# Kernel tuning notes

Measured on AMD Instinct MI355X. Metric: run time of the kernel, lower is better.

## Reference

```python
import jax, jax.numpy as jnp
import numpy as np

HEAD_NUM = 16
KEY_DIM = 64
EMBED = 1024
KV_OUT = HEAD_NUM * KEY_DIM  # 1024


def setup_inputs() -> dict:
    key = jax.random.key(0)
    ks = jax.random.split(key, 11)
    B, L, E = 2, 2048, EMBED
    scale = 0.02
    return {
        "query": jax.random.normal(ks[0], (B, L, E), jnp.float32),
        "key": jax.random.normal(ks[1], (B, L, E), jnp.float32),
        "value": jax.random.normal(ks[2], (B, L, E), jnp.float32),
        "W_Query": jax.random.normal(ks[3], (E, KV_OUT), jnp.float32) * scale,
        "W_Key": jax.random.normal(ks[4], (E, KV_OUT), jnp.float32) * scale,
        "W_Value": jax.random.normal(ks[5], (E, KV_OUT), jnp.float32) * scale,
        "W_Output": jax.random.normal(ks[6], (KV_OUT, E), jnp.float32) * scale,
        "B_Query": jnp.zeros((KV_OUT,), jnp.float32),
        "B_Key": jnp.zeros((KV_OUT,), jnp.float32),
        "B_Value": jnp.zeros((KV_OUT,), jnp.float32),
        "B_Output": jnp.zeros((E,), jnp.float32),
    }


def reference(query, key, value, W_Query, W_Key, W_Value, W_Output,
              B_Query, B_Key, B_Value, B_Output):
    B, Lq, E = query.shape
    Lk = key.shape[1]
    H, D = HEAD_NUM, KEY_DIM
    # QKV projections + bias
    q = query @ W_Query + B_Query            # [B, Lq, H*D]
    k = key @ W_Key + B_Key                  # [B, Lk, H*D]
    v = value @ W_Value + B_Value            # [B, Lk, H*D]
    # tf.split(axis=2) per head == reshape to [B, L, H, D]
    q = q.reshape(B, Lq, H, D)
    k = k.reshape(B, Lk, H, D)
    v = v.reshape(B, Lk, H, D)
    # scaled dot-product attention (no mask, dropout=0)
    scores = jnp.einsum("bqhd,bkhd->bhqk", q, k) / (D ** 0.5)
    probs = jax.nn.softmax(scores, axis=-1)
    out = jnp.einsum("bhqk,bkhd->bqhd", probs, v)  # [B, Lq, H, D]
    out = out.reshape(B, Lq, H * D)
    return out @ W_Output + B_Output
```

## Files before the change

### kernel.cpp

```cpp
#include <hip/hip_runtime.h>

using u16 = unsigned short;
using u32 = unsigned int;

typedef __attribute__((ext_vector_type(8))) short bf16x8;
typedef __attribute__((ext_vector_type(4))) float f32x4;
typedef __attribute__((ext_vector_type(4))) u32 u32x4;
typedef __attribute__((ext_vector_type(2))) u32 u32x2;
typedef __attribute__((ext_vector_type(4))) _Float16 f16x4;

#define MFMA_BF16_K32(a, b, c) __builtin_amdgcn_mfma_f32_16x16x32_bf16((a), (b), (c), 0, 0, 0)
#define MFMA_F16_K16(a, b, c) __builtin_amdgcn_mfma_f32_16x16x16f16((a), (b), (c), 0, 0, 0)

#define QSCALE 0.18033688011112042f

extern "C" __device__ float __ocml_native_exp2_f32(float);

__device__ __forceinline__ u16 f2bf(float f) {
  u32 u = __builtin_bit_cast(u32, f);
  return (u16)((u + 0x7fffu + ((u >> 16) & 1u)) >> 16);
}

__device__ __forceinline__ u32 pk_f16(float a, float b) {
  auto v = __builtin_amdgcn_cvt_pkrtz(a, b);
  return __builtin_bit_cast(u32, v);
}

__device__ __forceinline__ void load_lds16(const void* g, void* l) {
  __builtin_amdgcn_global_load_lds((__attribute__((address_space(1))) void*)g,
                                   (__attribute__((address_space(3))) void*)l,
                                   16, 0, 0);
}

__global__ __launch_bounds__(256) void cvt_all_kernel(
    const float* __restrict__ q, const float* __restrict__ k, const float* __restrict__ v,
    u16* __restrict__ oq, u16* __restrict__ ok, u16* __restrict__ ov,
    const float* __restrict__ w0, const float* __restrict__ w1,
    const float* __restrict__ w2, const float* __restrict__ w3,
    u16* __restrict__ d0, u16* __restrict__ d1,
    u16* __restrict__ d2, u16* __restrict__ d3) {
  const int id = blockIdx.x;
  const int tid = threadIdx.x;
  if (id < 6144) {
    const int z = id >> 11, bx = id & 2047;
    const float* s = z == 0 ? q : z == 1 ? k : v;
    u16* d = z == 0 ? oq : z == 1 ? ok : ov;
    int i = (bx * 256 + tid) * 8;
    f32x4 a = *(const f32x4*)(s + i);
    f32x4 b = *(const f32x4*)(s + i + 4);
    u32x4 o;
    o.x = (u32)f2bf(a.x) | ((u32)f2bf(a.y) << 16);
    o.y = (u32)f2bf(a.z) | ((u32)f2bf(a.w) << 16);
    o.z = (u32)f2bf(b.x) | ((u32)f2bf(b.y) << 16);
    o.w = (u32)f2bf(b.z) | ((u32)f2bf(b.w) << 16);
    *(u32x4*)(d + i) = o;
    return;
  }
  __shared__ float t[64][65];
  const int r0 = id - 6144;
  const int z = r0 >> 8, rr0 = r0 & 255;
  const int bx = rr0 & 15, by = rr0 >> 4;
  const float* src = z == 0 ? w0 : z == 1 ? w1 : z == 2 ? w2 : w3;
  u16* dst = z == 0 ? d0 : z == 1 ? d1 : z == 2 ? d2 : d3;
  const float scale = (z == 0) ? QSCALE : 1.0f;
  const int r = tid >> 4, c4 = (tid & 15) * 4;
#pragma unroll
  for (int i = 0; i < 4; ++i) {
    int row = r + i * 16;
    f32x4 vv = *(const f32x4*)(src + (by * 64 + row) * 1024 + bx * 64 + c4);
    t[row][c4 + 0] = vv.x;
    t[row][c4 + 1] = vv.y;
    t[row][c4 + 2] = vv.z;
    t[row][c4 + 3] = vv.w;
  }
  __syncthreads();
  const int rw = tid >> 2, cc = (tid & 3) * 16;
  alignas(16) u16 tmp[16];
#pragma unroll
  for (int j = 0; j < 16; ++j) tmp[j] = f2bf(t[cc + j][rw] * scale);
  u32x4* outp = (u32x4*)(dst + (bx * 64 + rw) * 1024 + by * 64 + cc);
  outp[0] = *(const u32x4*)&tmp[0];
  outp[1] = *(const u32x4*)&tmp[8];
}

__global__ __launch_bounds__(256) void gemm_qkv_kernel(
    const u16* __restrict__ x0, const u16* __restrict__ x1, const u16* __restrict__ x2,
    const u16* __restrict__ w0, const u16* __restrict__ w1, const u16* __restrict__ w2,
    const float* __restrict__ b0, const float* __restrict__ b1, const float* __restrict__ b2,
    u16* __restrict__ c0, u16* __restrict__ c1, u16* __restrict__ vt) {
  __shared__ u16 As[128 * 64];
  __shared__ u16 Bs[128 * 64];
  const int z = blockIdx.z;
  const u16* A = z == 0 ? x0 : z == 1 ? x1 : x2;
  const u16* Bt = z == 0 ? w0 : z == 1 ? w1 : w2;
  const float* bias = z == 0 ? b0 : z == 1 ? b1 : b2;
  const float bscale = z == 0 ? QSCALE : 1.0f;
  const int tid = threadIdx.x;
  const int wave = tid >> 6, lane = tid & 63;
  const int l16 = lane & 15, quad = lane >> 4;
  const int wm = wave >> 1, wn = wave & 1;
  const int m0 = blockIdx.y * 128, n0 = blockIdx.x * 128;

  f32x4 acc[4][4];
  const f32x4 zf = {0.f, 0.f, 0.f, 0.f};
#pragma unroll
  for (int i = 0; i < 4; ++i)
#pragma unroll
    for (int j = 0; j < 4; ++j) acc[i][j] = zf;

  for (int kb = 0; kb < 1024; kb += 64) {
#pragma unroll
    for (int t = 0; t < 4; ++t) {
      int c = wave * 256 + t * 64 + lane;
      int row = c >> 3, c8 = c & 7;
      load_lds16(A + (m0 + row) * 1024 + kb + c8 * 8, &As[(wave * 256 + t * 64) * 8]);
    }
#pragma unroll
    for (int t = 0; t < 4; ++t) {
      int c = wave * 256 + t * 64 + lane;
      int row = c >> 3, c8 = c & 7;
      load_lds16(Bt + (n0 + row) * 1024 + kb + c8 * 8, &Bs[(wave * 256 + t * 64) * 8]);
    }
    asm volatile("s_waitcnt vmcnt(0)" ::: "memory");
    __syncthreads();
#pragma unroll
    for (int ks = 0; ks < 2; ++ks) {
      bf16x8 af[4], bfv[4];
#pragma unroll
      for (int mt = 0; mt < 4; ++mt)
        af[mt] = *(const bf16x8*)&As[(wm * 64 + mt * 16 + l16) * 64 + ks * 32 + quad * 8];
#pragma unroll
      for (int nt = 0; nt < 4; ++nt)
        bfv[nt] = *(const bf16x8*)&Bs[(wn * 64 + nt * 16 + l16) * 64 + ks * 32 + quad * 8];
#pragma unroll
      for (int mt = 0; mt < 4; ++mt)
#pragma unroll
        for (int nt = 0; nt < 4; ++nt) acc[mt][nt] = MFMA_BF16_K32(af[mt], bfv[nt], acc[mt][nt]);
    }
    __syncthreads();
  }

  float bv[4];
#pragma unroll
  for (int nt = 0; nt < 4; ++nt) bv[nt] = bias[n0 + wn * 64 + nt * 16 + l16] * bscale;
  if (z != 2) {
    u16* C = z == 0 ? c0 : c1;
#pragma unroll
    for (int mt = 0; mt < 4; ++mt)
#pragma unroll
      for (int nt = 0; nt < 4; ++nt)
#pragma unroll
        for (int r = 0; r < 4; ++r) {
          int row = m0 + wm * 64 + mt * 16 + quad * 4 + r;
          int col = n0 + wn * 64 + nt * 16 + l16;
          C[row * 1024 + col] = f2bf(acc[mt][nt][r] + bv[nt]);
        }
  } else {
#pragma unroll
    for (int mt = 0; mt < 4; ++mt)
#pragma unroll
      for (int nt = 0; nt < 4; ++nt)
#pragma unroll
        for (int r = 0; r < 4; ++r) {
          int row = m0 + wm * 64 + mt * 16 + quad * 4 + r;
          int col = n0 + wn * 64 + nt * 16 + l16;
          int bb = row >> 11, kv = row & 2047;
          _Float16 hv = (_Float16)(acc[mt][nt][r] + bv[nt]);
          vt[(bb * 1024 + col) * 2048 + kv] = __builtin_bit_cast(u16, hv);
        }
  }
}

__global__ __launch_bounds__(256) void gemm_out_kernel(const u16* __restrict__ A,
                                                       const u16* __restrict__ Bt,
                                                       const float* __restrict__ bias,
                                                       float* __restrict__ C) {
  __shared__ u16 As[64 * 64];
  __shared__ u16 Bs[128 * 64];
  const int tid = threadIdx.x;
  const int wave = tid >> 6, lane = tid & 63;
  const int l16 = lane & 15, quad = lane >> 4;
  const int m0 = blockIdx.y * 64, n0 = blockIdx.x * 128;

  f32x4 acc[4][2];
  const f32x4 zf = {0.f, 0.f, 0.f, 0.f};
#pragma unroll
  for (int i = 0; i < 4; ++i)
#pragma unroll
    for (int j = 0; j < 2; ++j) acc[i][j] = zf;

  for (int kb = 0; kb < 1024; kb += 64) {
#pragma unroll
    for (int t = 0; t < 2; ++t) {
      int c = wave * 128 + t * 64 + lane;
      int row = c >> 3, c8 = c & 7;
      load_lds16(A + (m0 + row) * 1024 + kb + c8 * 8, &As[(wave * 128 + t * 64) * 8]);
    }
#pragma unroll
    for (int t = 0; t < 4; ++t) {
      int c = wave * 256 + t * 64 + lane;
      int row = c >> 3, c8 = c & 7;
      load_lds16(Bt + (n0 + row) * 1024 + kb + c8 * 8, &Bs[(wave * 256 + t * 64) * 8]);
    }
    asm volatile("s_waitcnt vmcnt(0)" ::: "memory");
    __syncthreads();
#pragma unroll
    for (int ks = 0; ks < 2; ++ks) {
      bf16x8 af[4], bfv[2];
#pragma unroll
      for (int mt = 0; mt < 4; ++mt)
        af[mt] = *(const bf16x8*)&As[(mt * 16 + l16) * 64 + ks * 32 + quad * 8];
#pragma unroll
      for (int nt = 0; nt < 2; ++nt)
        bfv[nt] = *(const bf16x8*)&Bs[(wave * 32 + nt * 16 + l16) * 64 + ks * 32 + quad * 8];
#pragma unroll
      for (int mt = 0; mt < 4; ++mt)
#pragma unroll
        for (int nt = 0; nt < 2; ++nt) acc[mt][nt] = MFMA_BF16_K32(af[mt], bfv[nt], acc[mt][nt]);
    }
    __syncthreads();
  }

  float bv[2];
#pragma unroll
  for (int nt = 0; nt < 2; ++nt) bv[nt] = bias[n0 + wave * 32 + nt * 16 + l16];
#pragma unroll
  for (int mt = 0; mt < 4; ++mt)
#pragma unroll
    for (int nt = 0; nt < 2; ++nt)
#pragma unroll
      for (int r = 0; r < 4; ++r) {
        int row = m0 + mt * 16 + quad * 4 + r;
        int col = n0 + wave * 32 + nt * 16 + l16;
        C[row * 1024 + col] = acc[mt][nt][r] + bv[nt];
      }
}

__global__ __launch_bounds__(256, 4) void flash_kernel(const u16* __restrict__ Q,
                                                       const u16* __restrict__ K,
                                                       const u16* __restrict__ Vt,
                                                       u16* __restrict__ O) {
  __shared__ u16 k_lds[128 * 72];
  __shared__ u16 vt_lds[64 * 132];
  const int tid = threadIdx.x;
  const int wave = tid >> 6, lane = tid & 63;
  const int l16 = lane & 15, quad = lane >> 4;
  const int id = blockIdx.x;
  const int xcd = id & 7, slot = id >> 3;
  const int pair = xcd * 4 + (slot & 3);
  const int qb = slot >> 2;
  const int b = pair >> 4, h = pair & 15;
  const u16* Qh = Q + (b * 2048 + qb * 64) * 1024 + h * 64;
  const u16* Kh = K + b * 2048 * 1024 + h * 64;
  const u16* Vh = Vt + pair * 64 * 2048;

  const int k_row[4] = {(0 * 256 + tid) >> 3, (1 * 256 + tid) >> 3,
                        (2 * 256 + tid) >> 3, (3 * 256 + tid) >> 3};
  const int k_c8 = (tid & 7) * 8;
  const int v_d[4] = {(0 * 256 + tid) >> 4, (1 * 256 + tid) >> 4,
                      (2 * 256 + tid) >> 4, (3 * 256 + tid) >> 4};
  const int v_c = (tid & 15) * 8;

  u32x4 kcur[4], vcur[4], knxt[4], vnxt[4];
#pragma unroll
  for (int t = 0; t < 4; ++t) {
    kcur[t] = *(const u32x4*)(Kh + k_row[t] * 1024 + k_c8);
    vcur[t] = *(const u32x4*)(Vh + v_d[t] * 2048 + v_c);
  }

#pragma unroll
  for (int t = 0; t < 2; ++t) {
    int idx = t * 256 + tid, row = idx >> 3, c8 = (idx & 7) * 8;
    *(u32x4*)&k_lds[row * 72 + c8] = *(const u32x4*)(Qh + row * 1024 + c8);
  }
  __syncthreads();
  bf16x8 qf[2];
#pragma unroll
  for (int ks = 0; ks < 2; ++ks)
    qf[ks] = *(const bf16x8*)&k_lds[(wave * 16 + l16) * 72 + ks * 32 + quad * 8];
  __syncthreads();

  f32x4 o_acc[4];
  const f32x4 zf = {0.f, 0.f, 0.f, 0.f};
#pragma unroll
  for (int dt = 0; dt < 4; ++dt) o_acc[dt] = zf;
  float lp = 0.f;

  for (int kb = 0; kb < 16; ++kb) {
#pragma unroll
    for (int t = 0; t < 4; ++t)
      *(u32x4*)&k_lds[k_row[t] * 72 + k_c8] = kcur[t];
#pragma unroll
    for (int t = 0; t < 4; ++t) {
      u32x2 vlo = {vcur[t].x, vcur[t].y}, vhi = {vcur[t].z, vcur[t].w};
      *(u32x2*)&vt_lds[v_d[t] * 132 + v_c] = vlo;
      *(u32x2*)&vt_lds[v_d[t] * 132 + v_c + 4] = vhi;
    }
    if (kb < 15) {
      const int kv1 = (kb + 1) * 128;
#pragma unroll
      for (int t = 0; t < 4; ++t) {
        knxt[t] = *(const u32x4*)(Kh + (kv1 + k_row[t]) * 1024 + k_c8);
        vnxt[t] = *(const u32x4*)(Vh + v_d[t] * 2048 + kv1 + v_c);
      }
    }
    __syncthreads();

#pragma unroll
    for (int chunk = 0; chunk < 8; ++chunk) {
      f32x4 s = zf;
#pragma unroll
      for (int ks = 0; ks < 2; ++ks) {
        bf16x8 kf = *(const bf16x8*)&k_lds[(chunk * 16 + l16) * 72 + ks * 32 + quad * 8];
        s = MFMA_BF16_K32(kf, qf[ks], s);
      }
      float e0 = __ocml_native_exp2_f32(s.x), e1 = __ocml_native_exp2_f32(s.y);
      float e2 = __ocml_native_exp2_f32(s.z), e3 = __ocml_native_exp2_f32(s.w);
      lp += (e0 + e1) + (e2 + e3);
      union { u32 u[2]; f16x4 v; } pk;
      pk.u[0] = pk_f16(e0, e1);
      pk.u[1] = pk_f16(e2, e3);
#pragma unroll
      for (int dt = 0; dt < 4; ++dt) {
        f16x4 vf = *(const f16x4*)&vt_lds[(dt * 16 + l16) * 132 + chunk * 16 + quad * 4];
        o_acc[dt] = MFMA_F16_K16(pk.v, vf, o_acc[dt]);
      }
    }
    __syncthreads();
#pragma unroll
    for (int t = 0; t < 4; ++t) {
      kcur[t] = knxt[t];
      vcur[t] = vnxt[t];
    }
  }

  lp += __shfl_xor(lp, 16);
  lp += __shfl_xor(lp, 32);
#pragma unroll
  for (int r = 0; r < 4; ++r) {
    float inv = 1.0f / __shfl(lp, quad * 4 + r);
    int row = b * 2048 + qb * 64 + wave * 16 + quad * 4 + r;
#pragma unroll
    for (int dt = 0; dt < 4; ++dt)
      O[row * 1024 + h * 64 + dt * 16 + l16] = f2bf(o_acc[dt][r] * inv);
  }
}

extern "C" void kernel_launch(void* const* d_in, const int* in_sizes, int n_in,
                              void* d_out, int out_size, void* d_ws, size_t ws_size,
                              hipStream_t stream) {
  const float* q = (const float*)d_in[0];
  const float* k = (const float*)d_in[1];
  const float* v = (const float*)d_in[2];
  const float* Wq = (const float*)d_in[3];
  const float* Wk = (const float*)d_in[4];
  const float* Wv = (const float*)d_in[5];
  const float* Wo = (const float*)d_in[6];
  const float* Bq = (const float*)d_in[7];
  const float* Bk = (const float*)d_in[8];
  const float* Bv = (const float*)d_in[9];
  const float* Bo = (const float*)d_in[10];
  float* out = (float*)d_out;

  char* w = (char*)d_ws;
  const size_t MB = 1u << 20;
  u16* xq = (u16*)(w + 0 * MB);
  u16* xk = (u16*)(w + 8 * MB);
  u16* xv = (u16*)(w + 16 * MB);
  u16* wqt = (u16*)(w + 24 * MB);
  u16* wkt = (u16*)(w + 26 * MB);
  u16* wvt = (u16*)(w + 28 * MB);
  u16* wot = (u16*)(w + 30 * MB);
  u16* Qp = (u16*)(w + 32 * MB);
  u16* Kp = (u16*)(w + 40 * MB);
  u16* Vtr = (u16*)(w + 48 * MB);
  u16* At = (u16*)(w + 56 * MB);

  cvt_all_kernel<<<dim3(7168), 256, 0, stream>>>(q, k, v, xq, xk, xv,
                                                 Wq, Wk, Wv, Wo, wqt, wkt, wvt, wot);
  gemm_qkv_kernel<<<dim3(8, 32, 3), 256, 0, stream>>>(xq, xk, xv, wqt, wkt, wvt,
                                                      Bq, Bk, Bv, Qp, Kp, Vtr);
  flash_kernel<<<dim3(1024), 256, 0, stream>>>(Qp, Kp, Vtr, At);
  gemm_out_kernel<<<dim3(8, 64), 256, 0, stream>>>(At, wot, Bo, out);
}
```

Before: 250.0 us.

## Swizzle LDS tiles with XOR and remap GEMM blocks for XCD locality

After: 230.6 us. 1.08x faster.

```diff
diff --git a/kernel.cpp b/kernel.cpp
--- a/kernel.cpp
+++ b/kernel.cpp
@@ -90,7 +90,11 @@
     u16* __restrict__ c0, u16* __restrict__ c1, u16* __restrict__ vt) {
   __shared__ u16 As[128 * 64];
   __shared__ u16 Bs[128 * 64];
-  const int z = blockIdx.z;
+  const int lid = blockIdx.x;
+  const int xcd = lid & 7, rr = lid >> 3;
+  const int nb = rr & 7, slot = rr >> 3;
+  const int g = slot * 8 + xcd;
+  const int z = g >> 5, m_idx = g & 31;
   const u16* A = z == 0 ? x0 : z == 1 ? x1 : x2;
   const u16* Bt = z == 0 ? w0 : z == 1 ? w1 : w2;
   const float* bias = z == 0 ? b0 : z == 1 ? b1 : b2;
@@ -98,8 +102,9 @@
   const int tid = threadIdx.x;
   const int wave = tid >> 6, lane = tid & 63;
   const int l16 = lane & 15, quad = lane >> 4;
+  const int l7 = l16 & 7;
   const int wm = wave >> 1, wn = wave & 1;
-  const int m0 = blockIdx.y * 128, n0 = blockIdx.x * 128;
+  const int m0 = m_idx * 128, n0 = nb * 128;
 
   f32x4 acc[4][4];
   const f32x4 zf = {0.f, 0.f, 0.f, 0.f};
@@ -112,26 +117,27 @@
 #pragma unroll
     for (int t = 0; t < 4; ++t) {
       int c = wave * 256 + t * 64 + lane;
-      int row = c >> 3, c8 = c & 7;
-      load_lds16(A + (m0 + row) * 1024 + kb + c8 * 8, &As[(wave * 256 + t * 64) * 8]);
+      int row = c >> 3, sc8 = (c & 7) ^ (row & 7);
+      load_lds16(A + (m0 + row) * 1024 + kb + sc8 * 8, &As[(wave * 256 + t * 64) * 8]);
     }
 #pragma unroll
     for (int t = 0; t < 4; ++t) {
       int c = wave * 256 + t * 64 + lane;
-      int row = c >> 3, c8 = c & 7;
-      load_lds16(Bt + (n0 + row) * 1024 + kb + c8 * 8, &Bs[(wave * 256 + t * 64) * 8]);
+      int row = c >> 3, sc8 = (c & 7) ^ (row & 7);
+      load_lds16(Bt + (n0 + row) * 1024 + kb + sc8 * 8, &Bs[(wave * 256 + t * 64) * 8]);
     }
     asm volatile("s_waitcnt vmcnt(0)" ::: "memory");
     __syncthreads();
 #pragma unroll
     for (int ks = 0; ks < 2; ++ks) {
+      const int sch = (ks * 4 + quad) ^ l7;
       bf16x8 af[4], bfv[4];
 #pragma unroll
       for (int mt = 0; mt < 4; ++mt)
-        af[mt] = *(const bf16x8*)&As[(wm * 64 + mt * 16 + l16) * 64 + ks * 32 + quad * 8];
+        af[mt] = *(const bf16x8*)&As[(wm * 64 + mt * 16 + l16) * 64 + sch * 8];
 #pragma unroll
       for (int nt = 0; nt < 4; ++nt)
-        bfv[nt] = *(const bf16x8*)&Bs[(wn * 64 + nt * 16 + l16) * 64 + ks * 32 + quad * 8];
+        bfv[nt] = *(const bf16x8*)&Bs[(wn * 64 + nt * 16 + l16) * 64 + sch * 8];
 #pragma unroll
       for (int mt = 0; mt < 4; ++mt)
 #pragma unroll
@@ -177,10 +183,15 @@
                                                        float* __restrict__ C) {
   __shared__ u16 As[64 * 64];
   __shared__ u16 Bs[128 * 64];
+  const int lid = blockIdx.x;
+  const int xcd = lid & 7, rr = lid >> 3;
+  const int nb = rr & 7, slot = rr >> 3;
+  const int by = slot * 8 + xcd;
   const int tid = threadIdx.x;
   const int wave = tid >> 6, lane = tid & 63;
   const int l16 = lane & 15, quad = lane >> 4;
-  const int m0 = blockIdx.y * 64, n0 = blockIdx.x * 128;
+  const int l7 = l16 & 7;
+  const int m0 = by * 64, n0 = nb * 128;
 
   f32x4 acc[4][2];
   const f32x4 zf = {0.f, 0.f, 0.f, 0.f};
@@ -193,26 +204,27 @@
 #pragma unroll
     for (int t = 0; t < 2; ++t) {
       int c = wave * 128 + t * 64 + lane;
-      int row = c >> 3, c8 = c & 7;
-      load_lds16(A + (m0 + row) * 1024 + kb + c8 * 8, &As[(wave * 128 + t * 64) * 8]);
+      int row = c >> 3, sc8 = (c & 7) ^ (row & 7);
+      load_lds16(A + (m0 + row) * 1024 + kb + sc8 * 8, &As[(wave * 128 + t * 64) * 8]);
     }
 #pragma unroll
     for (int t = 0; t < 4; ++t) {
       int c = wave * 256 + t * 64 + lane;
-      int row = c >> 3, c8 = c & 7;
-      load_lds16(Bt + (n0 + row) * 1024 + kb + c8 * 8, &Bs[(wave * 256 + t * 64) * 8]);
+      int row = c >> 3, sc8 = (c & 7) ^ (row & 7);
+      load_lds16(Bt + (n0 + row) * 1024 + kb + sc8 * 8, &Bs[(wave * 256 + t * 64) * 8]);
     }
     asm volatile("s_waitcnt vmcnt(0)" ::: "memory");
     __syncthreads();
 #pragma unroll
     for (int ks = 0; ks < 2; ++ks) {
+      const int sch = (ks * 4 + quad) ^ l7;
       bf16x8 af[4], bfv[2];
 #pragma unroll
       for (int mt = 0; mt < 4; ++mt)
-        af[mt] = *(const bf16x8*)&As[(mt * 16 + l16) * 64 + ks * 32 + quad * 8];
+        af[mt] = *(const bf16x8*)&As[(mt * 16 + l16) * 64 + sch * 8];
 #pragma unroll
       for (int nt = 0; nt < 2; ++nt)
-        bfv[nt] = *(const bf16x8*)&Bs[(wave * 32 + nt * 16 + l16) * 64 + ks * 32 + quad * 8];
+        bfv[nt] = *(const bf16x8*)&Bs[(wave * 32 + nt * 16 + l16) * 64 + sch * 8];
 #pragma unroll
       for (int mt = 0; mt < 4; ++mt)
 #pragma unroll
@@ -378,8 +390,8 @@
 
   cvt_all_kernel<<<dim3(7168), 256, 0, stream>>>(q, k, v, xq, xk, xv,
                                                  Wq, Wk, Wv, Wo, wqt, wkt, wvt, wot);
-  gemm_qkv_kernel<<<dim3(8, 32, 3), 256, 0, stream>>>(xq, xk, xv, wqt, wkt, wvt,
-                                                      Bq, Bk, Bv, Qp, Kp, Vtr);
+  gemm_qkv_kernel<<<dim3(768), 256, 0, stream>>>(xq, xk, xv, wqt, wkt, wvt,
+                                                 Bq, Bk, Bv, Qp, Kp, Vtr);
   flash_kernel<<<dim3(1024), 256, 0, stream>>>(Qp, Kp, Vtr, At);
-  gemm_out_kernel<<<dim3(8, 64), 256, 0, stream>>>(At, wot, Bo, out);
-}
+  gemm_out_kernel<<<dim3(512), 256, 0, stream>>>(At, wot, Bo, out);
+}
```
